# Performance work log

Measured on AMD Instinct MI355X. Metric: run time of the kernel, lower is better.

## Reference

```python
import jax, jax.numpy as jnp
import numpy as np

B, C, H, W = 8, 64, 256, 256


def setup_inputs() -> dict:
    key = jax.random.key(0)
    ks = jax.random.split(key, 7)
    return {
        "x": jax.random.normal(ks[0], (B, C, H, W), dtype=jnp.float32),
        "query_w": jax.random.normal(ks[1], (C, W, W), dtype=jnp.float32),
        "key_w": jax.random.normal(ks[2], (C, W, W), dtype=jnp.float32),
        "var_w": jax.random.normal(ks[3], (C, W, W), dtype=jnp.float32),
        "query_b": jax.random.normal(ks[4], (C, H, W), dtype=jnp.float32),
        "key_b": jax.random.normal(ks[5], (C, H, W), dtype=jnp.float32),
        "var_b": jax.random.normal(ks[6], (C, H, W), dtype=jnp.float32),
    }


def reference(x, query_w, key_w, var_w, query_b, key_b, var_b):
    # mode == 'horizontal': per-channel right-matmul over the W axis.
    # x: [B,C,H,W], *_w: [C,W,W] (broadcast over batch), *_b: [C,H,W].
    q = jnp.einsum("bchw,cwv->bchv", x, query_w) + query_b
    k = jnp.einsum("bchw,cwv->bchv", x, key_w) + key_b
    v = jnp.einsum("bchw,cwv->bchv", x, var_w) + var_b
    return jax.nn.softmax(q * k, axis=-1) * v
```

## Files before the change

kernel.cpp:

```cpp
#include <hip/hip_runtime.h>
#include <math.h>


#define Bn 8
#define Cn 64
#define Hn 256
#define Wn 256

typedef _Float16 f16x8 __attribute__((ext_vector_type(8)));
typedef _Float16 f16x4 __attribute__((ext_vector_type(4)));
typedef float    f32x16 __attribute__((ext_vector_type(16)));

#define MFMA(a, b, c) __builtin_amdgcn_mfma_f32_32x32x16_f16((a), (b), (c), 0, 0, 0)

#define LDS_ALO 2048
#define LDS_B   4096
#define LDS_SM  36864

__global__ __launch_bounds__(256, 2) void axile_attn_mfma3(
    const float* __restrict__ x,
    const float* __restrict__ wq,
    const float* __restrict__ wk,
    const float* __restrict__ wv,
    const float* __restrict__ bq,
    const float* __restrict__ bk,
    const float* __restrict__ bv,
    float* __restrict__ out)
{
    __shared__ __align__(16) char lds[38400];

    const int tid  = threadIdx.x;
    const int ncol = tid >> 6;
    const int lane = tid & 63;
    const int h    = lane >> 5;
    const int l31  = lane & 31;

    const int blk = blockIdx.x;
    const int c   = blk & 63;
    const int j   = blk >> 6;
    const int b   = j >> 2;
    const int h0  = (j & 3) * 64;

    const float* xbase = x + ((size_t)(b * Cn + c) * Hn + h0) * Wn;
    const float* w_q = wq + (size_t)c * Wn * Wn;
    const float* w_k = wk + (size_t)c * Wn * Wn;
    const float* w_v = wv + (size_t)c * Wn * Wn;

    const int n    = tid;
    const int ntW  = n >> 5;
    const int nl   = n & 31;
    const int am    = tid >> 2;
    const int akq   = tid & 3;
    const int amt   = am >> 5;
    const int alc   = ((akq >> 1) << 5) | (am & 31);
    const int aboff = (akq & 1) * 8;

    f32x16 accq[2][2], acck[2][2];
#pragma unroll
    for (int mt = 0; mt < 2; ++mt)
#pragma unroll
        for (int nt = 0; nt < 2; ++nt)
#pragma unroll
            for (int r = 0; r < 16; ++r) {
                accq[mt][nt][r] = 0.f;
                acck[mt][nt][r] = 0.f;
            }

    for (int kt = 0; kt < 16; ++kt) {
        const int k0 = kt * 16;
        __syncthreads();
#pragma unroll
        for (int mat = 0; mat < 2; ++mat) {
            const float* Wp = mat ? w_k : w_q;
            float w16[16];
#pragma unroll
            for (int r = 0; r < 16; ++r)
                w16[r] = Wp[(size_t)(k0 + r) * Wn + n];
            char* dplane = lds + LDS_B + (mat * 2) * 8192 + ntW * 1024;
#pragma unroll
            for (int h2 = 0; h2 < 2; ++h2) {
                f16x8 hi8, lo8;
#pragma unroll
                for (int e = 0; e < 8; ++e) {
                    const float wv_ = w16[h2 * 8 + e];
                    _Float16 hv = (_Float16)wv_;
                    hi8[e] = hv;
                    lo8[e] = (_Float16)(wv_ - (float)hv);
                }
                const int fo = ((h2 << 5) | nl) * 16;
                *(f16x8*)(dplane + fo) = hi8;
                *(f16x8*)(dplane + 8192 + fo) = lo8;
            }
        }
        {
            const float4 xx = *(const float4*)(xbase + (size_t)am * Wn + k0 + akq * 4);
            f16x4 hi4, lo4;
            _Float16 t0 = (_Float16)xx.x; hi4[0] = t0; lo4[0] = (_Float16)(xx.x - (float)t0);
            _Float16 t1 = (_Float16)xx.y; hi4[1] = t1; lo4[1] = (_Float16)(xx.y - (float)t1);
            _Float16 t2 = (_Float16)xx.z; hi4[2] = t2; lo4[2] = (_Float16)(xx.z - (float)t2);
            _Float16 t3 = (_Float16)xx.w; hi4[3] = t3; lo4[3] = (_Float16)(xx.w - (float)t3);
            *(f16x4*)(lds + amt * 1024 + alc * 16 + aboff) = hi4;
            *(f16x4*)(lds + LDS_ALO + amt * 1024 + alc * 16 + aboff) = lo4;
        }
        __syncthreads();

        f16x8 ah[2], al[2];
#pragma unroll
        for (int mt = 0; mt < 2; ++mt) {
            ah[mt] = *(const f16x8*)(lds + mt * 1024 + lane * 16);
            al[mt] = *(const f16x8*)(lds + LDS_ALO + mt * 1024 + lane * 16);
        }
#pragma unroll
        for (int nt = 0; nt < 2; ++nt) {
            const int ntile = ncol * 2 + nt;
            const char* bb = lds + LDS_B + ntile * 1024 + lane * 16;
            f16x8 bqh = *(const f16x8*)(bb + 0 * 8192);
            f16x8 bql = *(const f16x8*)(bb + 1 * 8192);
            f16x8 bkh = *(const f16x8*)(bb + 2 * 8192);
            f16x8 bkl = *(const f16x8*)(bb + 3 * 8192);
#pragma unroll
            for (int mt = 0; mt < 2; ++mt) {
                accq[mt][nt] = MFMA(ah[mt], bqh, accq[mt][nt]);
                accq[mt][nt] = MFMA(al[mt], bqh, accq[mt][nt]);
                accq[mt][nt] = MFMA(ah[mt], bql, accq[mt][nt]);
                acck[mt][nt] = MFMA(ah[mt], bkh, acck[mt][nt]);
                acck[mt][nt] = MFMA(al[mt], bkh, acck[mt][nt]);
                acck[mt][nt] = MFMA(ah[mt], bkl, acck[mt][nt]);
            }
        }
    }

    float* part    = (float*)(lds + LDS_SM);
    float* combmax = (float*)(lds + LDS_SM + 1024);
    float* combsum = (float*)(lds + LDS_SM + 1280);

#pragma unroll
    for (int mt = 0; mt < 2; ++mt)
#pragma unroll
        for (int nt = 0; nt < 2; ++nt)
#pragma unroll
            for (int r = 0; r < 16; ++r) {
                const int rl = (r & 3) + 8 * (r >> 2) + 4 * h;
                const int hh = h0 + mt * 32 + rl;
                const int vv = ncol * 64 + nt * 32 + l31;
                const size_t bidx = ((size_t)c * Hn + hh) * Wn + vv;
                const float qv = accq[mt][nt][r] + bq[bidx];
                const float kv = acck[mt][nt][r] + bk[bidx];
                accq[mt][nt][r] = qv * kv;
            }

#pragma unroll
    for (int mt = 0; mt < 2; ++mt)
#pragma unroll
        for (int r = 0; r < 16; ++r) {
            float m2 = fmaxf(accq[mt][0][r], accq[mt][1][r]);
#pragma unroll
            for (int off = 16; off > 0; off >>= 1)
                m2 = fmaxf(m2, __shfl_xor(m2, off, 64));
            if ((lane & 15) == r && ((lane >> 4) & 1) == mt) {
                const int rl  = (r & 3) + 8 * (r >> 2) + 4 * h;
                const int row = mt * 32 + rl;
                part[row * 4 + ncol] = m2;
            }
        }
    __syncthreads();
    if (tid < 64)
        combmax[tid] = fmaxf(fmaxf(part[tid * 4 + 0], part[tid * 4 + 1]),
                             fmaxf(part[tid * 4 + 2], part[tid * 4 + 3]));
    __syncthreads();

#pragma unroll
    for (int mt = 0; mt < 2; ++mt)
#pragma unroll
        for (int r = 0; r < 16; ++r) {
            const int rl  = (r & 3) + 8 * (r >> 2) + 4 * h;
            const int row = mt * 32 + rl;
            const float mx = combmax[row];
            const float e0 = __expf(accq[mt][0][r] - mx);
            const float e1 = __expf(accq[mt][1][r] - mx);
            accq[mt][0][r] = e0;
            accq[mt][1][r] = e1;
            float ps = e0 + e1;
#pragma unroll
            for (int off = 16; off > 0; off >>= 1)
                ps += __shfl_xor(ps, off, 64);
            if ((lane & 15) == r && ((lane >> 4) & 1) == mt)
                part[row * 4 + ncol] = ps;
        }
    __syncthreads();
    if (tid < 64)
        combsum[tid] = (part[tid * 4 + 0] + part[tid * 4 + 1]) +
                       (part[tid * 4 + 2] + part[tid * 4 + 3]);

    f32x16 accv[2][2];
#pragma unroll
    for (int mt = 0; mt < 2; ++mt)
#pragma unroll
        for (int nt = 0; nt < 2; ++nt)
#pragma unroll
            for (int r = 0; r < 16; ++r)
                accv[mt][nt][r] = 0.f;

    for (int kt = 0; kt < 16; ++kt) {
        const int k0 = kt * 16;
        __syncthreads();
        {
            float w16[16];
#pragma unroll
            for (int r = 0; r < 16; ++r)
                w16[r] = w_v[(size_t)(k0 + r) * Wn + n];
            char* dplane = lds + LDS_B + ntW * 1024;
#pragma unroll
            for (int h2 = 0; h2 < 2; ++h2) {
                f16x8 hi8;
#pragma unroll
                for (int e = 0; e < 8; ++e)
                    hi8[e] = (_Float16)w16[h2 * 8 + e];
                *(f16x8*)(dplane + ((h2 << 5) | nl) * 16) = hi8;
            }
        }
        {
            const float4 xx = *(const float4*)(xbase + (size_t)am * Wn + k0 + akq * 4);
            f16x4 hi4;
            hi4[0] = (_Float16)xx.x;
            hi4[1] = (_Float16)xx.y;
            hi4[2] = (_Float16)xx.z;
            hi4[3] = (_Float16)xx.w;
            *(f16x4*)(lds + amt * 1024 + alc * 16 + aboff) = hi4;
        }
        __syncthreads();

        f16x8 ah[2];
#pragma unroll
        for (int mt = 0; mt < 2; ++mt)
            ah[mt] = *(const f16x8*)(lds + mt * 1024 + lane * 16);
#pragma unroll
        for (int nt = 0; nt < 2; ++nt) {
            const int ntile = ncol * 2 + nt;
            f16x8 bvh = *(const f16x8*)(lds + LDS_B + ntile * 1024 + lane * 16);
#pragma unroll
            for (int mt = 0; mt < 2; ++mt)
                accv[mt][nt] = MFMA(ah[mt], bvh, accv[mt][nt]);
        }
    }

    float* obase = out + ((size_t)(b * Cn + c) * Hn) * Wn;
#pragma unroll
    for (int mt = 0; mt < 2; ++mt)
#pragma unroll
        for (int r = 0; r < 16; ++r) {
            const int rl  = (r & 3) + 8 * (r >> 2) + 4 * h;
            const int row = mt * 32 + rl;
            const float inv = 1.0f / combsum[row];
            const int hh = h0 + row;
#pragma unroll
            for (int nt = 0; nt < 2; ++nt) {
                const int vv = ncol * 64 + nt * 32 + l31;
                const size_t bidx = ((size_t)c * Hn + hh) * Wn + vv;
                const float vx = accv[mt][nt][r] + bv[bidx];
                obase[(size_t)hh * Wn + vv] = accq[mt][nt][r] * vx * inv;
            }
        }
}

extern "C" void kernel_launch(void* const* d_in, const int* in_sizes, int n_in,
                              void* d_out, int out_size, void* d_ws, size_t ws_size,
                              hipStream_t stream) {
    (void)in_sizes; (void)n_in; (void)out_size; (void)d_ws; (void)ws_size;
    const float* x  = (const float*)d_in[0];
    const float* wq = (const float*)d_in[1];
    const float* wk = (const float*)d_in[2];
    const float* wv = (const float*)d_in[3];
    const float* bq = (const float*)d_in[4];
    const float* bk = (const float*)d_in[5];
    const float* bv = (const float*)d_in[6];
    float* out = (float*)d_out;

    dim3 grid(Bn * 4 * Cn);
    dim3 block(256);
    hipLaunchKernelGGL(axile_attn_mfma3, grid, block, 0, stream,
                       x, wq, wk, wv, bq, bk, bv, out);
}
```

Before: 534.8 us.

## Double block to 512 threads, one 32-column tile per wave

Block size goes from 256 to 512 threads, so each of eight waves owns one 32-column N tile instead of two. This halves the accumulator registers per thread to allow higher occupancy. Weight staging is split across thread halves, with each staging 8 of the 16 K rows, and the softmax cross-wave reduction is widened to eight partials. More waves share each barrier, and the x staging still uses only half the threads.

```diff
diff --git a/kernel.cpp b/kernel.cpp
--- a/kernel.cpp
+++ b/kernel.cpp
@@ -17,7 +17,7 @@
 #define LDS_B   4096
 #define LDS_SM  36864
 
-__global__ __launch_bounds__(256, 2) void axile_attn_mfma3(
+__global__ __launch_bounds__(512, 4) void axile_attn_mfma4(
     const float* __restrict__ x,
     const float* __restrict__ wq,
     const float* __restrict__ wk,
@@ -27,7 +27,7 @@
     const float* __restrict__ bv,
     float* __restrict__ out)
 {
-    __shared__ __align__(16) char lds[38400];
+    __shared__ __align__(16) char lds[39424];
 
     const int tid  = threadIdx.x;
     const int ncol = tid >> 6;
@@ -46,25 +46,25 @@
     const float* w_k = wk + (size_t)c * Wn * Wn;
     const float* w_v = wv + (size_t)c * Wn * Wn;
 
-    const int n    = tid;
-    const int ntW  = n >> 5;
-    const int nl   = n & 31;
+    const int wkh = tid >> 8;
+    const int n   = tid & 255;
+    const int ntW = n >> 5;
+    const int nl  = n & 31;
+    const int wfo = ((wkh << 5) | nl) * 16;
     const int am    = tid >> 2;
     const int akq   = tid & 3;
     const int amt   = am >> 5;
     const int alc   = ((akq >> 1) << 5) | (am & 31);
     const int aboff = (akq & 1) * 8;
 
-    f32x16 accq[2][2], acck[2][2];
-#pragma unroll
-    for (int mt = 0; mt < 2; ++mt)
-#pragma unroll
-        for (int nt = 0; nt < 2; ++nt)
-#pragma unroll
-            for (int r = 0; r < 16; ++r) {
-                accq[mt][nt][r] = 0.f;
-                acck[mt][nt][r] = 0.f;
-            }
+    f32x16 accq[2], acck[2];
+#pragma unroll
+    for (int mt = 0; mt < 2; ++mt)
+#pragma unroll
+        for (int r = 0; r < 16; ++r) {
+            accq[mt][r] = 0.f;
+            acck[mt][r] = 0.f;
+        }
 
     for (int kt = 0; kt < 16; ++kt) {
         const int k0 = kt * 16;
@@ -72,27 +72,24 @@
 #pragma unroll
         for (int mat = 0; mat < 2; ++mat) {
             const float* Wp = mat ? w_k : w_q;
-            float w16[16];
-#pragma unroll
-            for (int r = 0; r < 16; ++r)
-                w16[r] = Wp[(size_t)(k0 + r) * Wn + n];
+            const float* wrow = Wp + (size_t)(k0 + wkh * 8) * Wn + n;
+            float w8[8];
+#pragma unroll
+            for (int r = 0; r < 8; ++r)
+                w8[r] = wrow[(size_t)r * Wn];
+            f16x8 hi8, lo8;
+#pragma unroll
+            for (int e = 0; e < 8; ++e) {
+                const float wv_ = w8[e];
+                _Float16 hv = (_Float16)wv_;
+                hi8[e] = hv;
+                lo8[e] = (_Float16)(wv_ - (float)hv);
+            }
             char* dplane = lds + LDS_B + (mat * 2) * 8192 + ntW * 1024;
-#pragma unroll
-            for (int h2 = 0; h2 < 2; ++h2) {
-                f16x8 hi8, lo8;
-#pragma unroll
-                for (int e = 0; e < 8; ++e) {
-                    const float wv_ = w16[h2 * 8 + e];
-                    _Float16 hv = (_Float16)wv_;
-                    hi8[e] = hv;
-                    lo8[e] = (_Float16)(wv_ - (float)hv);
-                }
-                const int fo = ((h2 << 5) | nl) * 16;
-                *(f16x8*)(dplane + fo) = hi8;
-                *(f16x8*)(dplane + 8192 + fo) = lo8;
-            }
-        }
-        {
+            *(f16x8*)(dplane + wfo) = hi8;
+            *(f16x8*)(dplane + 8192 + wfo) = lo8;
+        }
+        if (tid < 256) {
             const float4 xx = *(const float4*)(xbase + (size_t)am * Wn + k0 + akq * 4);
             f16x4 hi4, lo4;
             _Float16 t0 = (_Float16)xx.x; hi4[0] = t0; lo4[0] = (_Float16)(xx.x - (float)t0);
@@ -110,63 +107,61 @@
             ah[mt] = *(const f16x8*)(lds + mt * 1024 + lane * 16);
             al[mt] = *(const f16x8*)(lds + LDS_ALO + mt * 1024 + lane * 16);
         }
-#pragma unroll
-        for (int nt = 0; nt < 2; ++nt) {
-            const int ntile = ncol * 2 + nt;
-            const char* bb = lds + LDS_B + ntile * 1024 + lane * 16;
-            f16x8 bqh = *(const f16x8*)(bb + 0 * 8192);
-            f16x8 bql = *(const f16x8*)(bb + 1 * 8192);
-            f16x8 bkh = *(const f16x8*)(bb + 2 * 8192);
-            f16x8 bkl = *(const f16x8*)(bb + 3 * 8192);
-#pragma unroll
-            for (int mt = 0; mt < 2; ++mt) {
-                accq[mt][nt] = MFMA(ah[mt], bqh, accq[mt][nt]);
-                accq[mt][nt] = MFMA(al[mt], bqh, accq[mt][nt]);
-                accq[mt][nt] = MFMA(ah[mt], bql, accq[mt][nt]);
-                acck[mt][nt] = MFMA(ah[mt], bkh, acck[mt][nt]);
-                acck[mt][nt] = MFMA(al[mt], bkh, acck[mt][nt]);
-                acck[mt][nt] = MFMA(ah[mt], bkl, acck[mt][nt]);
-            }
+        const char* bb = lds + LDS_B + ncol * 1024 + lane * 16;
+        f16x8 bqh = *(const f16x8*)(bb + 0 * 8192);
+        f16x8 bql = *(const f16x8*)(bb + 1 * 8192);
+        f16x8 bkh = *(const f16x8*)(bb + 2 * 8192);
+        f16x8 bkl = *(const f16x8*)(bb + 3 * 8192);
+#pragma unroll
+        for (int mt = 0; mt < 2; ++mt) {
+            accq[mt] = MFMA(ah[mt], bqh, accq[mt]);
+            accq[mt] = MFMA(al[mt], bqh, accq[mt]);
+            accq[mt] = MFMA(ah[mt], bql, accq[mt]);
+            acck[mt] = MFMA(ah[mt], bkh, acck[mt]);
+            acck[mt] = MFMA(al[mt], bkh, acck[mt]);
+            acck[mt] = MFMA(ah[mt], bkl, acck[mt]);
         }
     }
 
     float* part    = (float*)(lds + LDS_SM);
-    float* combmax = (float*)(lds + LDS_SM + 1024);
-    float* combsum = (float*)(lds + LDS_SM + 1280);
-
-#pragma unroll
-    for (int mt = 0; mt < 2; ++mt)
-#pragma unroll
-        for (int nt = 0; nt < 2; ++nt)
-#pragma unroll
-            for (int r = 0; r < 16; ++r) {
-                const int rl = (r & 3) + 8 * (r >> 2) + 4 * h;
-                const int hh = h0 + mt * 32 + rl;
-                const int vv = ncol * 64 + nt * 32 + l31;
-                const size_t bidx = ((size_t)c * Hn + hh) * Wn + vv;
-                const float qv = accq[mt][nt][r] + bq[bidx];
-                const float kv = acck[mt][nt][r] + bk[bidx];
-                accq[mt][nt][r] = qv * kv;
-            }
-
-#pragma unroll
-    for (int mt = 0; mt < 2; ++mt)
-#pragma unroll
-        for (int r = 0; r < 16; ++r) {
-            float m2 = fmaxf(accq[mt][0][r], accq[mt][1][r]);
+    float* combmax = (float*)(lds + LDS_SM + 2048);
+    float* combsum = (float*)(lds + LDS_SM + 2304);
+
+#pragma unroll
+    for (int mt = 0; mt < 2; ++mt)
+#pragma unroll
+        for (int r = 0; r < 16; ++r) {
+            const int rl = (r & 3) + 8 * (r >> 2) + 4 * h;
+            const int hh = h0 + mt * 32 + rl;
+            const int vv = ncol * 32 + l31;
+            const size_t bidx = ((size_t)c * Hn + hh) * Wn + vv;
+            const float qv = accq[mt][r] + bq[bidx];
+            const float kv = acck[mt][r] + bk[bidx];
+            accq[mt][r] = qv * kv;
+        }
+
+#pragma unroll
+    for (int mt = 0; mt < 2; ++mt)
+#pragma unroll
+        for (int r = 0; r < 16; ++r) {
+            float m2 = accq[mt][r];
 #pragma unroll
             for (int off = 16; off > 0; off >>= 1)
                 m2 = fmaxf(m2, __shfl_xor(m2, off, 64));
             if ((lane & 15) == r && ((lane >> 4) & 1) == mt) {
                 const int rl  = (r & 3) + 8 * (r >> 2) + 4 * h;
                 const int row = mt * 32 + rl;
-                part[row * 4 + ncol] = m2;
+                part[ncol * 64 + row] = m2;
             }
         }
     __syncthreads();
-    if (tid < 64)
-        combmax[tid] = fmaxf(fmaxf(part[tid * 4 + 0], part[tid * 4 + 1]),
-                             fmaxf(part[tid * 4 + 2], part[tid * 4 + 3]));
+    if (tid < 64) {
+        float m = part[tid];
+#pragma unroll
+        for (int w = 1; w < 8; ++w)
+            m = fmaxf(m, part[w * 64 + tid]);
+        combmax[tid] = m;
+    }
     __syncthreads();
 
 #pragma unroll
@@ -176,50 +171,47 @@
             const int rl  = (r & 3) + 8 * (r >> 2) + 4 * h;
             const int row = mt * 32 + rl;
             const float mx = combmax[row];
-            const float e0 = __expf(accq[mt][0][r] - mx);
-            const float e1 = __expf(accq[mt][1][r] - mx);
-            accq[mt][0][r] = e0;
-            accq[mt][1][r] = e1;
-            float ps = e0 + e1;
+            const float e0 = __expf(accq[mt][r] - mx);
+            accq[mt][r] = e0;
+            float ps = e0;
 #pragma unroll
             for (int off = 16; off > 0; off >>= 1)
                 ps += __shfl_xor(ps, off, 64);
             if ((lane & 15) == r && ((lane >> 4) & 1) == mt)
-                part[row * 4 + ncol] = ps;
+                part[ncol * 64 + row] = ps;
         }
     __syncthreads();
-    if (tid < 64)
-        combsum[tid] = (part[tid * 4 + 0] + part[tid * 4 + 1]) +
-                       (part[tid * 4 + 2] + part[tid * 4 + 3]);
-
-    f32x16 accv[2][2];
-#pragma unroll
-    for (int mt = 0; mt < 2; ++mt)
-#pragma unroll
-        for (int nt = 0; nt < 2; ++nt)
-#pragma unroll
-            for (int r = 0; r < 16; ++r)
-                accv[mt][nt][r] = 0.f;
+    if (tid < 64) {
+        float s = part[tid];
+#pragma unroll
+        for (int w = 1; w < 8; ++w)
+            s += part[w * 64 + tid];
+        combsum[tid] = s;
+    }
+
+    f32x16 accv[2];
+#pragma unroll
+    for (int mt = 0; mt < 2; ++mt)
+#pragma unroll
+        for (int r = 0; r < 16; ++r)
+            accv[mt][r] = 0.f;
 
     for (int kt = 0; kt < 16; ++kt) {
         const int k0 = kt * 16;
         __syncthreads();
         {
-            float w16[16];
-#pragma unroll
-            for (int r = 0; r < 16; ++r)
-                w16[r] = w_v[(size_t)(k0 + r) * Wn + n];
-            char* dplane = lds + LDS_B + ntW * 1024;
-#pragma unroll
-            for (int h2 = 0; h2 < 2; ++h2) {
-                f16x8 hi8;
-#pragma unroll
-                for (int e = 0; e < 8; ++e)
-                    hi8[e] = (_Float16)w16[h2 * 8 + e];
-                *(f16x8*)(dplane + ((h2 << 5) | nl) * 16) = hi8;
-            }
-        }
-        {
+            const float* wrow = w_v + (size_t)(k0 + wkh * 8) * Wn + n;
+            float w8[8];
+#pragma unroll
+            for (int r = 0; r < 8; ++r)
+                w8[r] = wrow[(size_t)r * Wn];
+            f16x8 hi8;
+#pragma unroll
+            for (int e = 0; e < 8; ++e)
+                hi8[e] = (_Float16)w8[e];
+            *(f16x8*)(lds + LDS_B + ntW * 1024 + wfo) = hi8;
+        }
+        if (tid < 256) {
             const float4 xx = *(const float4*)(xbase + (size_t)am * Wn + k0 + akq * 4);
             f16x4 hi4;
             hi4[0] = (_Float16)xx.x;
@@ -234,14 +226,10 @@
 #pragma unroll
         for (int mt = 0; mt < 2; ++mt)
             ah[mt] = *(const f16x8*)(lds + mt * 1024 + lane * 16);
-#pragma unroll
-        for (int nt = 0; nt < 2; ++nt) {
-            const int ntile = ncol * 2 + nt;
-            f16x8 bvh = *(const f16x8*)(lds + LDS_B + ntile * 1024 + lane * 16);
-#pragma unroll
-            for (int mt = 0; mt < 2; ++mt)
-                accv[mt][nt] = MFMA(ah[mt], bvh, accv[mt][nt]);
-        }
+        f16x8 bvh = *(const f16x8*)(lds + LDS_B + ncol * 1024 + lane * 16);
+#pragma unroll
+        for (int mt = 0; mt < 2; ++mt)
+            accv[mt] = MFMA(ah[mt], bvh, accv[mt]);
     }
 
     float* obase = out + ((size_t)(b * Cn + c) * Hn) * Wn;
@@ -253,13 +241,10 @@
             const int row = mt * 32 + rl;
             const float inv = 1.0f / combsum[row];
             const int hh = h0 + row;
-#pragma unroll
-            for (int nt = 0; nt < 2; ++nt) {
-                const int vv = ncol * 64 + nt * 32 + l31;
-                const size_t bidx = ((size_t)c * Hn + hh) * Wn + vv;
-                const float vx = accv[mt][nt][r] + bv[bidx];
-                obase[(size_t)hh * Wn + vv] = accq[mt][nt][r] * vx * inv;
-            }
+            const int vv = ncol * 32 + l31;
+            const size_t bidx = ((size_t)c * Hn + hh) * Wn + vv;
+            const float vx = accv[mt][r] + bv[bidx];
+            obase[(size_t)hh * Wn + vv] = accq[mt][r] * vx * inv;
         }
 }
 
@@ -277,7 +262,7 @@
     float* out = (float*)d_out;
 
     dim3 grid(Bn * 4 * Cn);
-    dim3 block(256);
-    hipLaunchKernelGGL(axile_attn_mfma3, grid, block, 0, stream,
+    dim3 block(512);
+    hipLaunchKernelGGL(axile_attn_mfma4, grid, block, 0, stream,
                        x, wq, wk, wv, bq, bk, bv, out);
 }
```

Result: no change. 530.2 us (-0.9%).
